# Kernel tuning notes

Hardware: AMD Instinct MI355X
Metric: run time of the kernel (lower is better)

The kernel has to match this reference:

```python
import jax, jax.numpy as jnp
import numpy as np

H = 20   # num heads
D = 64   # head dim (hidden_size=1280)
N_IMG = 4
N_LBL = 4
SCALE_IMG = 1.0
SCALE_LBL = 1.0


def setup_inputs() -> dict:
    key = jax.random.key(0)
    ks = jax.random.split(key, 12)
    B, S, C, Dc = 4, 4096, 1280, 2048
    L = 77 + N_IMG + N_LBL  # 85 encoder tokens
    w = lambda k, shp: jax.random.normal(k, shp, dtype=jnp.float32) * 0.02
    return {
        "hidden_states": jax.random.normal(ks[0], (B, S, C), dtype=jnp.float32),
        "encoder_hidden_states": jax.random.normal(ks[1], (B, L, Dc), dtype=jnp.float32),
        "Wq": w(ks[2], (C, C)),
        "Wk": w(ks[3], (Dc, C)),
        "Wv": w(ks[4], (Dc, C)),
        "Wk_ip": w(ks[5], (Dc, C)),
        "Wv_ip": w(ks[6], (Dc, C)),
        "Wk_lbl": w(ks[7], (Dc, C)),
        "Wv_lbl": w(ks[8], (Dc, C)),
        "Wo": w(ks[9], (C, C)),
        "bo": jnp.zeros((C,), dtype=jnp.float32),
    }


def _attend(q, enc, Wk_, Wv_):
    # q: [B, S, H, D]; enc: [B, L, Dc]
    B, L = enc.shape[0], enc.shape[1]
    k = (enc @ Wk_).reshape(B, L, H, D)
    v = (enc @ Wv_).reshape(B, L, H, D)
    scores = jnp.einsum("bqhd,bkhd->bhqk", q, k) * (D ** -0.5)
    p = jax.nn.softmax(scores, axis=-1)
    return jnp.einsum("bhqk,bkhd->bqhd", p, v)


def reference(hidden_states, encoder_hidden_states, Wq, Wk, Wv,
              Wk_ip, Wv_ip, Wk_lbl, Wv_lbl, Wo, bo):
    B, S, C = hidden_states.shape
    end = encoder_hidden_states.shape[1] - N_IMG - N_LBL
    enc_text = encoder_hidden_states[:, :end]
    enc_img = encoder_hidden_states[:, end:end + N_IMG]
    enc_lbl = encoder_hidden_states[:, end + N_IMG:]

    q = (hidden_states @ Wq).reshape(B, S, H, D)

    out = _attend(q, enc_text, Wk, Wv)
    out = out + SCALE_IMG * _attend(q, enc_img, Wk_ip, Wv_ip)
    out = out + SCALE_LBL * _attend(q, enc_lbl, Wk_lbl, Wv_lbl)

    out = out.reshape(B, S, C) @ Wo + bo
    return out + hidden_states  # residual_connection=True, rescale=1.0
```

## Files before the change

### kernel.cpp

```cpp
#include <hip/hip_runtime.h>
#include <hip/hip_bf16.h>

typedef unsigned short u16;
using f32x4  = __attribute__((ext_vector_type(4))) float;
using bf16x8 = __attribute__((ext_vector_type(8))) short;

#define N_B 4
#define N_S 4096
#define N_C 1280
#define N_DC 2048
#define N_H 20
#define N_D 64

__device__ __forceinline__ u16 f2b(float f) {
  union { float f; unsigned u; } x; x.f = f;
  return (u16)((x.u + 0x7fffu + ((x.u >> 16) & 1u)) >> 16);
}

__device__ __forceinline__ void gld16(const u16* g, u16* l) {
  __builtin_amdgcn_global_load_lds(
      (const __attribute__((address_space(1))) unsigned int*)(g),
      (__attribute__((address_space(3))) unsigned int*)(l), 16, 0, 0);
}

struct TPargs { const float* s[8]; u16* d[8]; int K[8]; };

__device__ __forceinline__ void tp_tile(const float* __restrict__ src,
                                        u16* __restrict__ dst, int K,
                                        int n0, int k0, int t, char* smem) {
  float (*tl)[65] = (float(*)[65])smem;
  int r = t >> 4, c4 = (t & 15) * 4;
#pragma unroll
  for (int j = 0; j < 8; j++) {
    float4 v4 = *(const float4*)(src + (size_t)(k0 + j * 16 + r) * N_C + n0 + c4);
    tl[j * 16 + r][c4]     = v4.x;
    tl[j * 16 + r][c4 + 1] = v4.y;
    tl[j * 16 + r][c4 + 2] = v4.z;
    tl[j * 16 + r][c4 + 3] = v4.w;
  }
  __syncthreads();
  int n = t >> 4, koff = (t & 15) * 8;
#pragma unroll
  for (int j = 0; j < 4; j++) {
    int nn = j * 16 + n;
    alignas(16) u16 tmp[8];
#pragma unroll
    for (int kk = 0; kk < 8; kk++) tmp[kk] = f2b(tl[koff + kk][nn]);
    *(uint4*)(dst + (size_t)(n0 + nn) * K + k0 + koff) = *(uint4*)tmp;
  }
}

__global__ __launch_bounds__(256)
void k_prep(TPargs a, const float* __restrict__ enc, u16* __restrict__ txt,
            u16* __restrict__ img, u16* __restrict__ lbl) {
  __shared__ __align__(16) char smem[33280];
  int bx = blockIdx.x, t = threadIdx.x;
  if (bx < 2240) {
    int z = bx / 320, v = bx % 320;
    int n0 = (v % 20) * 64, k0 = (v / 20) * 128;
    int K = a.K[z];
    if (k0 >= K) return;
    tp_tile(a.s[z], a.d[z], K, n0, k0, t, smem);
  } else {
    int row = bx - 2240;
    int b = row / 85, l = row % 85;
    const float* s = enc + (size_t)row * N_DC;
    u16* d;
    if (l < 77)      d = txt + (size_t)(b * 77 + l) * N_DC;
    else if (l < 81) d = img + (size_t)(b * 4 + (l - 77)) * N_DC;
    else             d = lbl + (size_t)(b * 4 + (l - 81)) * N_DC;
    for (int i = t * 8; i < N_DC; i += 256 * 8) {
      const float4 v0 = *(const float4*)(s + i);
      const float4 v1 = *(const float4*)(s + i + 4);
      alignas(16) u16 tmp[8];
      tmp[0] = f2b(v0.x); tmp[1] = f2b(v0.y); tmp[2] = f2b(v0.z); tmp[3] = f2b(v0.w);
      tmp[4] = f2b(v1.x); tmp[5] = f2b(v1.y); tmp[6] = f2b(v1.z); tmp[7] = f2b(v1.w);
      *(uint4*)(d + i) = *(uint4*)tmp;
    }
  }
}

__global__ __launch_bounds__(256)
void k_cvt(const float* __restrict__ src, u16* __restrict__ dst, int n4) {
  for (int i = blockIdx.x * 256 + threadIdx.x; i < n4; i += 2048 * 256) {
    float4 v = ((const float4*)src)[i];
    union { u16 s[4]; uint2 u; } tmp;
    tmp.s[0] = f2b(v.x); tmp.s[1] = f2b(v.y);
    tmp.s[2] = f2b(v.z); tmp.s[3] = f2b(v.w);
    ((uint2*)dst)[i] = tmp.u;
  }
}

__device__ __forceinline__ void stage32(const u16* __restrict__ g, int ldK,
                                        int row0, int kk, u16* ldsb,
                                        int w, int lane) {
  int r = row0 + w * 8 + (lane >> 3);
  int gslot = ((lane & 7) ^ (lane >> 3)) << 3;
  gld16(g + (size_t)r * ldK + kk + gslot, ldsb + w * 512);
}
__device__ __forceinline__ void stageA(const u16* Ag, int K, int kk, u16* ldsb,
                                       int w, int lane) {
#pragma unroll
  for (int j = 0; j < 4; j++)
    stage32(Ag, K, j * 32, kk, ldsb + j * 2048, w, lane);
}
__device__ __forceinline__ void stageB(const u16* Bg, int K, int kk, u16* ldsb,
                                       int w, int lane) {
#pragma unroll
  for (int j = 0; j < 5; j++)
    stage32(Bg, K, j * 32, kk, ldsb + j * 2048, w, lane);
}

#define RD_A2(aoff, mh)                                                      \
  _Pragma("unroll") for (int mi = 0; mi < 2; mi++) {                         \
    _Pragma("unroll") for (int ks = 0; ks < 2; ks++) {                       \
      int row = wr * 64 + ((mh) * 2 + mi) * 16 + lrow;                       \
      int slot = (ks * 4 + g) ^ (lane & 7);                                  \
      af[mi][ks] = *(const bf16x8*)&lds[(aoff) + row * 64 + slot * 8];       \
    }                                                                        \
  }

#define RD_B5(boff)                                                          \
  _Pragma("unroll") for (int n = 0; n < 5; n++) {                            \
    _Pragma("unroll") for (int ks = 0; ks < 2; ks++) {                       \
      int row = wc * 80 + n * 16 + lrow;                                     \
      int slot = (ks * 4 + g) ^ (lane & 7);                                  \
      bf[n][ks] = *(const bf16x8*)&lds[(boff) + row * 64 + slot * 8];        \
    }                                                                        \
  }

#define MFMA10(mh)                                                           \
  _Pragma("unroll") for (int ks = 0; ks < 2; ks++) {                         \
    _Pragma("unroll") for (int n = 0; n < 5; n++)                            \
      acc[mh][n] = __builtin_amdgcn_mfma_f32_16x16x32_bf16(                  \
          af[(mh) & 1][ks], bf[n][ks], acc[mh][n], 0, 0, 0);                 \
  }

#define BARR()  __builtin_amdgcn_s_barrier()
#define VM0()   asm volatile("s_waitcnt vmcnt(0)" ::: "memory")
#define PRIO(x) __builtin_amdgcn_s_setprio(x)

template<int EPI>
__device__ __forceinline__ void gemm_body(
    const u16* __restrict__ A, const u16* __restrict__ Bt, void* __restrict__ Cv,
    int M, int N, int K, float scale,
    const float* __restrict__ bias, const float* __restrict__ resid,
    u16* lds, int bid, int nwg) {
  const int t = threadIdx.x, lane = t & 63, w = t >> 6;
  const int wr = w >> 1, wc = w & 1;
  const int lrow = lane & 15, g = lane >> 4;

  int nt = N / 160;
  int swz = ((nwg & 7) == 0) ? ((bid & 7) * (nwg >> 3) + (bid >> 3)) : bid;
  int bm = swz / nt, bn = swz % nt;

  const u16* Ag = A  + (size_t)bm * 128 * K;
  const u16* Bg = Bt + (size_t)bn * 160 * K;
  const int NT = K >> 6;

  f32x4 acc[4][5] = {};
  bf16x8 af[2][2], bf[5][2];

  stageA(Ag, K, 0, lds + 0,     w, lane);
  stageB(Bg, K, 0, lds + 16384, w, lane);
  VM0();
  BARR();

  for (int tt = 0; tt < NT; ++tt) {
    int c = tt & 1;
    int aof  = c * 8192,        bof  = 16384 + c * 10240;
    int aof1 = (c ^ 1) * 8192,  bof1 = 16384 + (c ^ 1) * 10240;
    if (tt + 1 < NT) {
      stageA(Ag, K, (tt + 1) * 64, lds + aof1, w, lane);
      stageB(Bg, K, (tt + 1) * 64, lds + bof1, w, lane);
    }
    RD_B5(bof);
    RD_A2(aof, 0);
    PRIO(1); MFMA10(0); MFMA10(1); PRIO(0);
    RD_A2(aof, 1);
    PRIO(1); MFMA10(2); MFMA10(3); PRIO(0);
    VM0();
    BARR();
  }

#pragma unroll
  for (int m = 0; m < 4; m++) {
    int row = bm * 128 + wr * 64 + m * 16 + g * 4;
#pragma unroll
    for (int n = 0; n < 5; n++) {
      int col = bn * 160 + wc * 80 + n * 16 + lrow;
#pragma unroll
      for (int j = 0; j < 4; j++) {
        float v = acc[m][n][j];
        if constexpr (EPI == 1)
          ((u16*)Cv)[(size_t)(row + j) * N + col] = f2b(v * scale);
        else
          ((float*)Cv)[(size_t)(row + j) * N + col] =
              v + bias[col] + resid[(size_t)(row + j) * N + col];
      }
    }
  }
}

__device__ __forceinline__ void kv_body(
    const u16* __restrict__ A, const u16* __restrict__ Bt, u16* __restrict__ C,
    int M, int bm, int bn, u16* ldsraw) {
  u16 (*lds)[2][8192] = (u16(*)[2][8192])ldsraw;
  const int K = 2048;
  int t = threadIdx.x, lane = t & 63, w = t >> 6;
  int wm = w >> 1, wn = w & 1;
  int gs = ((lane & 7) ^ (lane >> 3)) * 8;
  int rsub = lane >> 3;

  f32x4 acc[4][4] = {};

#define KVSTAGE(kt, buf)                                                      \
  {                                                                           \
    int k0 = (kt) * 64;                                                       \
    _Pragma("unroll") for (int i2 = 0; i2 < 4; i2++) {                        \
      int rloc = w * 32 + i2 * 8;                                             \
      int ra = bm * 128 + rloc + rsub; if (ra >= M) ra = M - 1;               \
      int rb = bn * 128 + rloc + rsub;                                        \
      gld16(A  + (size_t)ra * K + k0 + gs, &lds[buf][0][rloc * 64]);          \
      gld16(Bt + (size_t)rb * K + k0 + gs, &lds[buf][1][rloc * 64]);          \
    }                                                                         \
  }

  KVSTAGE(0, 0);
  VM0();
  __syncthreads();
  int cur = 0;
  for (int kt = 0; kt < 32; kt++) {
    if (kt < 31) KVSTAGE(kt + 1, cur ^ 1);
#pragma unroll
    for (int ks = 0; ks < 2; ks++) {
      bf16x8 afr[4], bfr[4];
#pragma unroll
      for (int m = 0; m < 4; m++) {
        int row = wm * 64 + m * 16 + (lane & 15);
        int slot = (ks * 4 + (lane >> 4)) ^ (lane & 7);
        afr[m] = *(bf16x8*)&lds[cur][0][row * 64 + slot * 8];
      }
#pragma unroll
      for (int n = 0; n < 4; n++) {
        int row = wn * 64 + n * 16 + (lane & 15);
        int slot = (ks * 4 + (lane >> 4)) ^ (lane & 7);
        bfr[n] = *(bf16x8*)&lds[cur][1][row * 64 + slot * 8];
      }
#pragma unroll
      for (int m = 0; m < 4; m++)
#pragma unroll
        for (int n = 0; n < 4; n++)
          acc[m][n] = __builtin_amdgcn_mfma_f32_16x16x32_bf16(afr[m], bfr[n], acc[m][n], 0, 0, 0);
    }
    VM0();
    __syncthreads();
    cur ^= 1;
  }
#undef KVSTAGE

#pragma unroll
  for (int m = 0; m < 4; m++) {
    int row = bm * 128 + wm * 64 + m * 16 + ((lane >> 4) << 2);
#pragma unroll
    for (int n = 0; n < 4; n++) {
      int col = bn * 128 + wn * 64 + n * 16 + (lane & 15);
#pragma unroll
      for (int j = 0; j < 4; j++) {
        int r = row + j;
        if (r >= M) continue;
        C[(size_t)r * 1280 + col] = f2b(acc[m][n][j]);
      }
    }
  }
}

__global__ __launch_bounds__(256, 2)
void qkv_gemm(const u16* __restrict__ hsb, const u16* __restrict__ wq,
              u16* __restrict__ qbuf,
              const u16* __restrict__ etxt, const u16* __restrict__ eimg,
              const u16* __restrict__ elbl,
              const u16* __restrict__ wk,   const u16* __restrict__ wv,
              const u16* __restrict__ wkip, const u16* __restrict__ wvip,
              const u16* __restrict__ wklb, const u16* __restrict__ wvlb,
              u16* ktxt, u16* vtxt, u16* kimg, u16* vimg, u16* klbl, u16* vlbl) {
  __shared__ __align__(16) u16 lds[36864];
  int bx = blockIdx.x;
  if (bx < 100) {
    int bn = bx % 10, my = (bx / 10) % 5, kv = bx / 50;
    const u16 *A, *Bt; u16* C; int M, bm;
    if (my < 3)       { A = etxt; M = 308; bm = my; Bt = kv ? wv   : wk;   C = kv ? vtxt : ktxt; }
    else if (my == 3) { A = eimg; M = 16;  bm = 0;  Bt = kv ? wvip : wkip; C = kv ? vimg : kimg; }
    else              { A = elbl; M = 16;  bm = 0;  Bt = kv ? wvlb : wklb; C = kv ? vlbl : klbl; }
    kv_body(A, Bt, C, M, bm, bn, lds);
  } else {
    gemm_body<1>(hsb, wq, qbuf, 16384, 1280, 1280, 0.125f, nullptr, nullptr,
                 lds, bx - 100, 1024);
  }
}

__global__ __launch_bounds__(256, 2)
void gemm_o(const u16* __restrict__ A, const u16* __restrict__ Bt,
            float* __restrict__ Cv, const float* __restrict__ bias,
            const float* __restrict__ resid) {
  __shared__ __align__(16) u16 lds[36864];
  gemm_body<2>(A, Bt, Cv, 16384, 1280, 1280, 1.f, bias, resid,
               lds, blockIdx.x, 1024);
}

#define QSTR 72
#define PSTR 104

__global__ __launch_bounds__(256, 2)
void attn_kern(const u16* __restrict__ q,
               const u16* __restrict__ ktxt, const u16* __restrict__ vtxt,
               const u16* __restrict__ kimg, const u16* __restrict__ vimg,
               const u16* __restrict__ klbl, const u16* __restrict__ vlbl,
               u16* __restrict__ outa,
               const float* __restrict__ Wo, u16* __restrict__ wo_t) {
  __shared__ __align__(16) char smem[45568];
  int bx = blockIdx.x;
  int t = threadIdx.x;
  if (bx >= 2560) {
    int v = bx - 2560;
    int n0 = (v % 20) * 64, k0 = (v / 20) * 128;
    tp_tile(Wo, wo_t, 1280, n0, k0, t, smem);
    return;
  }
  u16* Qs = (u16*)smem;
  u16* Ks = (u16*)(smem + 18432);
  u16* Ps = (u16*)smem;
  u16* Vt = (u16*)(smem + 32256);

  int st = bx & 31, h = (bx >> 5) % 20, b = bx / 640;
  int lane = t & 63, w = t >> 6;
  int s0 = st * 128;
  int c = lane & 15, g = lane >> 4;

  for (int i = t; i < 27136 / 16; i += 256)
    ((uint4*)(smem + 18432))[i] = make_uint4(0, 0, 0, 0);
#pragma unroll
  for (int i = 0; i < 4; i++) {
    int cid = t + i * 256; int r = cid >> 3, c8 = cid & 7;
    *(uint4*)&Qs[r * QSTR + c8 * 8] =
        *(const uint4*)(q + (size_t)(b * N_S + s0 + r) * N_C + h * N_D + c8 * 8);
  }
  __syncthreads();
  for (int cid = t; cid < 680; cid += 256) {
    int l = cid >> 3, c8 = cid & 7;
    const u16* p;
    if (l < 77)      p = ktxt + (size_t)(b * 77 + l) * N_C + h * N_D + c8 * 8;
    else if (l < 81) p = kimg + (size_t)(b * 4 + l - 77) * N_C + h * N_D + c8 * 8;
    else             p = klbl + (size_t)(b * 4 + l - 81) * N_C + h * N_D + c8 * 8;
    int row = (l < 77) ? l : l + 3;
    *(uint4*)&Ks[row * QSTR + c8 * 8] = *(const uint4*)p;
  }
  for (int e = t; e < 85 * 64; e += 256) {
    int l = e >> 6, d = e & 63;
    const u16* p;
    if (l < 77)      p = vtxt + (size_t)(b * 77 + l) * N_C + h * N_D + d;
    else if (l < 81) p = vimg + (size_t)(b * 4 + l - 77) * N_C + h * N_D + d;
    else             p = vlbl + (size_t)(b * 4 + l - 81) * N_C + h * N_D + d;
    int slot = (l < 77) ? l : l + 3;
    Vt[d * PSTR + slot] = *p;
  }
  __syncthreads();

  f32x4 sacc[2][6] = {};
#pragma unroll
  for (int ks = 0; ks < 2; ks++) {
    bf16x8 aq[2], bk[6];
#pragma unroll
    for (int m = 0; m < 2; m++)
      aq[m] = *(bf16x8*)&Qs[(w * 32 + m * 16 + c) * QSTR + ks * 32 + g * 8];
#pragma unroll
    for (int n = 0; n < 6; n++)
      bk[n] = *(bf16x8*)&Ks[(n * 16 + c) * QSTR + ks * 32 + g * 8];
#pragma unroll
    for (int m = 0; m < 2; m++)
#pragma unroll
      for (int n = 0; n < 6; n++)
        sacc[m][n] = __builtin_amdgcn_mfma_f32_16x16x32_bf16(aq[m], bk[n], sacc[m][n], 0, 0, 0);
  }
  __syncthreads();

  const float NEG = -1e30f;
#pragma unroll
  for (int m = 0; m < 2; m++) {
#pragma unroll
    for (int j = 0; j < 4; j++) {
      float tmax = NEG;
#pragma unroll
      for (int n = 0; n < 5; n++)
        if (n * 16 + c < 77) tmax = fmaxf(tmax, sacc[m][n][j]);
#pragma unroll
      for (int off = 1; off < 16; off <<= 1) tmax = fmaxf(tmax, __shfl_xor(tmax, off));
      float pv[5], tsum = 0.f;
#pragma unroll
      for (int n = 0; n < 5; n++) {
        float v = (n * 16 + c < 77) ? __expf(sacc[m][n][j] - tmax) : 0.f;
        pv[n] = v; tsum += v;
      }
#pragma unroll
      for (int off = 1; off < 16; off <<= 1) tsum += __shfl_xor(tsum, off);
      float v5 = sacc[m][5][j];
      float imax = (c < 4) ? v5 : NEG;
#pragma unroll
      for (int off = 1; off < 16; off <<= 1) imax = fmaxf(imax, __shfl_xor(imax, off));
      float ie = (c < 4) ? __expf(v5 - imax) : 0.f, isum = ie;
#pragma unroll
      for (int off = 1; off < 16; off <<= 1) isum += __shfl_xor(isum, off);
      float lmax = (c >= 4 && c < 8) ? v5 : NEG;
#pragma unroll
      for (int off = 1; off < 16; off <<= 1) lmax = fmaxf(lmax, __shfl_xor(lmax, off));
      float le = (c >= 4 && c < 8) ? __expf(v5 - lmax) : 0.f, lsum = le;
#pragma unroll
      for (int off = 1; off < 16; off <<= 1) lsum += __shfl_xor(lsum, off);

      float rt = 1.f / tsum;
      float p5 = (c < 4) ? ie / isum : ((c < 8) ? le / lsum : 0.f);
      int rowl = w * 32 + m * 16 + g * 4 + j;
#pragma unroll
      for (int n = 0; n < 5; n++)
        Ps[rowl * PSTR + n * 16 + c] = f2b(pv[n] * rt);
      Ps[rowl * PSTR + 80 + c] = f2b(p5);
    }
  }
  __syncthreads();

  f32x4 oacc[2][4] = {};
#pragma unroll
  for (int ks = 0; ks < 3; ks++) {
    bf16x8 ap[2], bv[4];
#pragma unroll
    for (int m = 0; m < 2; m++)
      ap[m] = *(bf16x8*)&Ps[(w * 32 + m * 16 + c) * PSTR + ks * 32 + g * 8];
#pragma unroll
    for (int n = 0; n < 4; n++)
      bv[n] = *(bf16x8*)&Vt[(n * 16 + c) * PSTR + ks * 32 + g * 8];
#pragma unroll
    for (int m = 0; m < 2; m++)
#pragma unroll
      for (int n = 0; n < 4; n++)
        oacc[m][n] = __builtin_amdgcn_mfma_f32_16x16x32_bf16(ap[m], bv[n], oacc[m][n], 0, 0, 0);
  }

#pragma unroll
  for (int m = 0; m < 2; m++) {
    int rbase = w * 32 + m * 16 + g * 4;
#pragma unroll
    for (int n = 0; n < 4; n++) {
      int d = n * 16 + c;
#pragma unroll
      for (int j = 0; j < 4; j++) {
        int s = s0 + rbase + j;
        outa[(size_t)(b * N_S + s) * N_C + h * N_D + d] = f2b(oacc[m][n][j]);
      }
    }
  }
}

extern "C" void kernel_launch(void* const* d_in, const int* in_sizes, int n_in,
                              void* d_out, int out_size, void* d_ws, size_t ws_size,
                              hipStream_t stream) {
  const float* hs   = (const float*)d_in[0];
  const float* enc  = (const float*)d_in[1];
  const float* Wq   = (const float*)d_in[2];
  const float* Wk   = (const float*)d_in[3];
  const float* Wv   = (const float*)d_in[4];
  const float* Wkip = (const float*)d_in[5];
  const float* Wvip = (const float*)d_in[6];
  const float* Wklb = (const float*)d_in[7];
  const float* Wvlb = (const float*)d_in[8];
  const float* Wo   = (const float*)d_in[9];
  const float* bo   = (const float*)d_in[10];

  if (ws_size < 83087360u) return;
  char* ws = (char*)d_ws;
  u16* wq_t   = (u16*)(ws + 0);
  u16* wo_t   = (u16*)(ws + 3276800);
  u16* wk_t   = (u16*)(ws + 6553600);
  u16* wv_t   = (u16*)(ws + 11796480);
  u16* wkip_t = (u16*)(ws + 17039360);
  u16* wvip_t = (u16*)(ws + 22282240);
  u16* wklb_t = (u16*)(ws + 27525120);
  u16* wvlb_t = (u16*)(ws + 32768000);
  u16* etxt   = (u16*)(ws + 38010880);
  u16* eimg   = (u16*)(ws + 39272448);
  u16* elbl   = (u16*)(ws + 39337984);
  u16* ktxt   = (u16*)(ws + 39403520);
  u16* vtxt   = (u16*)(ws + 40192000);
  u16* kimg   = (u16*)(ws + 40980480);
  u16* vimg   = (u16*)(ws + 41021440);
  u16* klbl   = (u16*)(ws + 41062400);
  u16* vlbl   = (u16*)(ws + 41103360);
  u16* attn   = (u16*)(ws + 41144320);
  u16* qbuf   = (u16*)d_out;
  u16* hsb    = (u16*)d_out + (size_t)N_S * N_B * N_C;

  TPargs tp;
  tp.s[0] = Wq;   tp.d[0] = wq_t;   tp.K[0] = 1280;
  tp.s[1] = Wk;   tp.d[1] = wk_t;   tp.K[1] = 2048;
  tp.s[2] = Wv;   tp.d[2] = wv_t;   tp.K[2] = 2048;
  tp.s[3] = Wkip; tp.d[3] = wkip_t; tp.K[3] = 2048;
  tp.s[4] = Wvip; tp.d[4] = wvip_t; tp.K[4] = 2048;
  tp.s[5] = Wklb; tp.d[5] = wklb_t; tp.K[5] = 2048;
  tp.s[6] = Wvlb; tp.d[6] = wvlb_t; tp.K[6] = 2048;
  tp.s[7] = Wo;   tp.d[7] = wo_t;   tp.K[7] = 1280;

  k_prep<<<2580, 256, 0, stream>>>(tp, enc, etxt, eimg, elbl);
  k_cvt<<<2048, 256, 0, stream>>>(hs, hsb, (N_B * N_S * N_C) / 4);

  qkv_gemm<<<1124, 256, 0, stream>>>(hsb, wq_t, qbuf,
                                     etxt, eimg, elbl,
                                     wk_t, wv_t, wkip_t, wvip_t, wklb_t, wvlb_t,
                                     ktxt, vtxt, kimg, vimg, klbl, vlbl);

  attn_kern<<<2760, 256, 0, stream>>>(qbuf, ktxt, vtxt, kimg, vimg,
                                      klbl, vlbl, attn, Wo, wo_t);

  gemm_o<<<1024, 256, 0, stream>>>(attn, wo_t, (float*)d_out, bo, hs);
}
```

Measured before the change: 222.2 us.

## Load Q fragments directly to registers, shrink LDS, raise attention occupancy

The attention kernel now reads Q MFMA fragments straight from global memory into registers instead of staging them through LDS. This shrinks the shared buffer and raises the launch-bounds occupancy hint from 2 to 4 blocks. The separate image and label softmax reductions are merged into one pair of 4-lane shuffle reductions, which cuts shuffle count. The risks are uncoalesced global Q loads and register pressure under the tighter occupancy bound.

```diff
diff --git a/kernel.cpp b/kernel.cpp
--- a/kernel.cpp
+++ b/kernel.cpp
@@ -311,14 +311,14 @@
 #define QSTR 72
 #define PSTR 104
 
-__global__ __launch_bounds__(256, 2)
+__global__ __launch_bounds__(256, 4)
 void attn_kern(const u16* __restrict__ q,
                const u16* __restrict__ ktxt, const u16* __restrict__ vtxt,
                const u16* __restrict__ kimg, const u16* __restrict__ vimg,
                const u16* __restrict__ klbl, const u16* __restrict__ vlbl,
                u16* __restrict__ outa,
                const float* __restrict__ Wo, u16* __restrict__ wo_t) {
-  __shared__ __align__(16) char smem[45568];
+  __shared__ __align__(16) char smem[39936];
   int bx = blockIdx.x;
   int t = threadIdx.x;
   if (bx >= 2560) {
@@ -327,24 +327,26 @@
     tp_tile(Wo, wo_t, 1280, n0, k0, t, smem);
     return;
   }
-  u16* Qs = (u16*)smem;
-  u16* Ks = (u16*)(smem + 18432);
+  u16* Ks = (u16*)smem;
   u16* Ps = (u16*)smem;
-  u16* Vt = (u16*)(smem + 32256);
+  u16* Vt = (u16*)(smem + 26624);
 
   int st = bx & 31, h = (bx >> 5) % 20, b = bx / 640;
   int lane = t & 63, w = t >> 6;
   int s0 = st * 128;
   int c = lane & 15, g = lane >> 4;
 
-  for (int i = t; i < 27136 / 16; i += 256)
-    ((uint4*)(smem + 18432))[i] = make_uint4(0, 0, 0, 0);
-#pragma unroll
-  for (int i = 0; i < 4; i++) {
-    int cid = t + i * 256; int r = cid >> 3, c8 = cid & 7;
-    *(uint4*)&Qs[r * QSTR + c8 * 8] =
-        *(const uint4*)(q + (size_t)(b * N_S + s0 + r) * N_C + h * N_D + c8 * 8);
-  }
+  bf16x8 aq[2][2];
+#pragma unroll
+  for (int m = 0; m < 2; m++)
+#pragma unroll
+    for (int ks = 0; ks < 2; ks++)
+      aq[m][ks] = *(const bf16x8*)(q +
+          (size_t)(b * N_S + s0 + w * 32 + m * 16 + c) * N_C + h * N_D +
+          ks * 32 + g * 8);
+
+  for (int i = t; i < 39936 / 16; i += 256)
+    ((uint4*)smem)[i] = make_uint4(0, 0, 0, 0);
   __syncthreads();
   for (int cid = t; cid < 680; cid += 256) {
     int l = cid >> 3, c8 = cid & 7;
@@ -369,10 +371,7 @@
   f32x4 sacc[2][6] = {};
 #pragma unroll
   for (int ks = 0; ks < 2; ks++) {
-    bf16x8 aq[2], bk[6];
-#pragma unroll
-    for (int m = 0; m < 2; m++)
-      aq[m] = *(bf16x8*)&Qs[(w * 32 + m * 16 + c) * QSTR + ks * 32 + g * 8];
+    bf16x8 bk[6];
 #pragma unroll
     for (int n = 0; n < 6; n++)
       bk[n] = *(bf16x8*)&Ks[(n * 16 + c) * QSTR + ks * 32 + g * 8];
@@ -380,7 +379,7 @@
     for (int m = 0; m < 2; m++)
 #pragma unroll
       for (int n = 0; n < 6; n++)
-        sacc[m][n] = __builtin_amdgcn_mfma_f32_16x16x32_bf16(aq[m], bk[n], sacc[m][n], 0, 0, 0);
+        sacc[m][n] = __builtin_amdgcn_mfma_f32_16x16x32_bf16(aq[m][ks], bk[n], sacc[m][n], 0, 0, 0);
   }
   __syncthreads();
 
@@ -404,21 +403,15 @@
 #pragma unroll
       for (int off = 1; off < 16; off <<= 1) tsum += __shfl_xor(tsum, off);
       float v5 = sacc[m][5][j];
-      float imax = (c < 4) ? v5 : NEG;
-#pragma unroll
-      for (int off = 1; off < 16; off <<= 1) imax = fmaxf(imax, __shfl_xor(imax, off));
-      float ie = (c < 4) ? __expf(v5 - imax) : 0.f, isum = ie;
-#pragma unroll
-      for (int off = 1; off < 16; off <<= 1) isum += __shfl_xor(isum, off);
-      float lmax = (c >= 4 && c < 8) ? v5 : NEG;
-#pragma unroll
-      for (int off = 1; off < 16; off <<= 1) lmax = fmaxf(lmax, __shfl_xor(lmax, off));
-      float le = (c >= 4 && c < 8) ? __expf(v5 - lmax) : 0.f, lsum = le;
-#pragma unroll
-      for (int off = 1; off < 16; off <<= 1) lsum += __shfl_xor(lsum, off);
-
+      float smax = (c < 8) ? v5 : NEG;
+      smax = fmaxf(smax, __shfl_xor(smax, 1));
+      smax = fmaxf(smax, __shfl_xor(smax, 2));
+      float se = (c < 8) ? __expf(v5 - smax) : 0.f;
+      float ssum = se;
+      ssum += __shfl_xor(ssum, 1);
+      ssum += __shfl_xor(ssum, 2);
       float rt = 1.f / tsum;
-      float p5 = (c < 4) ? ie / isum : ((c < 8) ? le / lsum : 0.f);
+      float p5 = (c < 8) ? se / ssum : 0.f;
       int rowl = w * 32 + m * 16 + g * 4 + j;
 #pragma unroll
       for (int n = 0; n < 5; n++)
```

After: 208.6 us. -6.2%, faster.
